# Optimization experiments

Hardware: AMD Instinct MI355X
Metric: run time of the kernel (lower is better)

The kernel has to match this reference:

```python
import jax, jax.numpy as jnp
import numpy as np

INPUT_SIZE = 1000
EMB = 1024          # 2**ceil(log2(input_size))
NQ = 10             # log2(EMB)
NL = 3              # n_qlayers (hardcoded in module)
B = 4096


def _rot(phi, theta, omega):
    # PennyLane qml.Rot(phi, theta, omega) = RZ(omega) RY(theta) RZ(phi)
    c = jnp.cos(theta * 0.5).astype(jnp.complex64)
    s = jnp.sin(theta * 0.5).astype(jnp.complex64)
    ea = jnp.exp(-0.5j * (phi + omega))   # e^{-i(phi+omega)/2}
    eb = jnp.exp(0.5j * (phi - omega))    # e^{ i(phi-omega)/2}
    row0 = jnp.stack([ea * c, -eb * s])
    row1 = jnp.stack([jnp.conj(eb) * s, jnp.conj(ea) * c])
    return jnp.stack([row0, row1])        # [2, 2] complex64


def _apply_1q(psi, U, q):
    # psi: [B] + [2]*NQ ; contract qubit axis q+1 with U
    psi = jnp.tensordot(psi, U, axes=[[q + 1], [1]])
    return jnp.moveaxis(psi, -1, q + 1)


def _apply_cnot(psi, c, t):
    c_ax, t_ax = c + 1, t + 1
    psi0 = jax.lax.index_in_dim(psi, 0, axis=c_ax, keepdims=False)
    psi1 = jax.lax.index_in_dim(psi, 1, axis=c_ax, keepdims=False)
    f_ax = t_ax - 1 if t_ax > c_ax else t_ax
    psi1 = jnp.flip(psi1, axis=f_ax)      # X on target when control=1
    return jnp.stack([psi0, psi1], axis=c_ax)


def _circuit(x, w):
    # AmplitudeEmbedding(normalize=True) + StronglyEntanglingLayers + probs
    norm = jnp.sqrt(jnp.sum(x * x, axis=1, keepdims=True))
    psi = (x / norm).astype(jnp.complex64)
    b = psi.shape[0]
    psi = psi.reshape((b,) + (2,) * NQ)   # wire 0 = most-significant bit
    for l in range(NL):
        for q in range(NQ):
            psi = _apply_1q(psi, _rot(w[l, q, 0], w[l, q, 1], w[l, q, 2]), q)
        r = l % (NQ - 1) + 1              # default SEL ranges
        for q in range(NQ):
            psi = _apply_cnot(psi, q, (q + r) % NQ)
    return (psi.real ** 2 + psi.imag ** 2).reshape(b, -1)  # probs [B, 2**NQ]


def setup_inputs() -> dict:
    key = jax.random.key(0)
    ks = jax.random.split(key, 12)
    d = {
        'inputs': jax.random.normal(ks[0], (B, INPUT_SIZE), jnp.float32),
        'weightsEnc': 0.1 * jax.random.normal(ks[1], (NL, NQ, 3), jnp.float32),
        'weightsDec': 0.1 * jax.random.normal(ks[2], (NL, NQ, 3), jnp.float32),
        'W0': jax.random.normal(ks[3], (INPUT_SIZE, EMB), jnp.float32) / np.sqrt(INPUT_SIZE),
        'b0': jnp.zeros((EMB,), jnp.float32),
        'W1': jax.random.normal(ks[4], (EMB, 2 * EMB), jnp.float32) / np.sqrt(EMB),
        'b1': jnp.zeros((2 * EMB,), jnp.float32),
        'W2': jax.random.normal(ks[5], (2 * EMB, EMB), jnp.float32) / np.sqrt(2 * EMB),
        'b2': jnp.zeros((EMB,), jnp.float32),
        'W3': jax.random.normal(ks[6], (EMB, INPUT_SIZE), jnp.float32) / np.sqrt(EMB),
        'b3': jnp.zeros((INPUT_SIZE,), jnp.float32),
    }
    return d


def reference(inputs, weightsEnc, weightsDec, W0, b0, W1, b1, W2, b2, W3, b3):
    x = inputs @ W0 + b0                 # Dense(embedding_dim)
    x = _circuit(x, weightsEnc)          # encoder qnode (vmapped over batch)
    x = x @ W1 + b1                      # Dense(2*embedding_dim)
    x = x @ W2 + b2                      # Dense(embedding_dim)
    x = _circuit(x, weightsDec)          # decoder qnode
    x = x @ W3 + b3                      # Dense(input_size)
    x = jnp.abs(x)
    return x / jnp.sum(x, axis=1, keepdims=True)
```

## Files before the change

kernel.cpp:

```cpp
#include <hip/hip_runtime.h>
#include <math.h>


#define B_SZ 4096
#define EMB 1024
#define NQ 10
#define NL 3

typedef __bf16 bf16x8 __attribute__((ext_vector_type(8)));
typedef float f32x4 __attribute__((ext_vector_type(4)));
typedef unsigned short u16x8 __attribute__((ext_vector_type(8)));

__device__ __forceinline__ unsigned short f2bf_rne(float f) {
    unsigned int u = __float_as_uint(f);
    u += 0x7FFFu + ((u >> 16) & 1u);
    return (unsigned short)(u >> 16);
}
__device__ __forceinline__ float bf2f(unsigned short h) {
    return __uint_as_float(((unsigned int)h) << 16);
}
__device__ __forceinline__ float lane_bcast(float v, int l) {
    return __uint_as_float(__builtin_amdgcn_readlane(__float_as_uint(v), l));
}

__device__ __forceinline__ void gll16(const void* g, void* l) {
    __builtin_amdgcn_global_load_lds(
        (const __attribute__((address_space(1))) void*)g,
        (__attribute__((address_space(3))) void*)l, 16, 0, 0);
}

#define GBM 128
#define GBN 128
#define GBK 32

__global__ __launch_bounds__(512) void gemm3_mfma(
    const unsigned short* __restrict__ Ah, const unsigned short* __restrict__ Al,
    const unsigned short* __restrict__ Bh, const unsigned short* __restrict__ Bl,
    const float* __restrict__ bias, float* __restrict__ C,
    int Kp, int Np, int Ksplit, size_t zStride)
{
    __shared__ __align__(16) char lds[32768];
    char* ldsAh = lds;
    char* ldsAl = lds + 8192;
    char* ldsBh = lds + 16384;
    char* ldsBl = lds + 24576;

    const int tid = threadIdx.x;
    const int lane = tid & 63;
    const int wv = tid >> 6;
    const int wm = wv >> 1;
    const int wn = wv & 1;
    const int blockRow = blockIdx.y * GBM;
    const int blockCol = blockIdx.x * GBN;
    const int z = blockIdx.z;

    const int srow = tid >> 2;
    const int skel = (tid & 3) * 8;
    const size_t aOff = ((size_t)(blockRow + srow) * Kp + skel + (size_t)z * Ksplit) * 2;
    const size_t bOff = ((size_t)(blockCol + srow) * Kp + skel + (size_t)z * Ksplit) * 2;
    const char* aHp = (const char*)Ah + aOff;
    const char* aLp = (const char*)Al + aOff;
    const char* bHp = (const char*)Bh + bOff;
    const char* bLp = (const char*)Bl + bOff;
    const int stageOff = wv * 1024;

    f32x4 acc[2][4];
    #pragma unroll
    for (int i = 0; i < 2; ++i)
        #pragma unroll
        for (int j = 0; j < 4; ++j)
            #pragma unroll
            for (int r = 0; r < 4; ++r) acc[i][j][r] = 0.f;

    const int kq = (lane >> 4) * 16;
    int aFragOff[2], bFragOff[4];
    #pragma unroll
    for (int i = 0; i < 2; ++i) aFragOff[i] = (wm * 32 + i * 16 + (lane & 15)) * 64 + kq;
    #pragma unroll
    for (int j = 0; j < 4; ++j) bFragOff[j] = (wn * 64 + j * 16 + (lane & 15)) * 64 + kq;

    const int nsteps = Ksplit / GBK;
    for (int s = 0; s < nsteps; ++s) {
        const size_t kb = (size_t)s * GBK * 2;
        gll16(aHp + kb, ldsAh + stageOff);
        gll16(aLp + kb, ldsAl + stageOff);
        gll16(bHp + kb, ldsBh + stageOff);
        gll16(bLp + kb, ldsBl + stageOff);
        __syncthreads();

        bf16x8 ah[2], al[2], bh[4], bl[4];
        #pragma unroll
        for (int i = 0; i < 2; ++i) {
            ah[i] = *(const bf16x8*)(ldsAh + aFragOff[i]);
            al[i] = *(const bf16x8*)(ldsAl + aFragOff[i]);
        }
        #pragma unroll
        for (int j = 0; j < 4; ++j) {
            bh[j] = *(const bf16x8*)(ldsBh + bFragOff[j]);
            bl[j] = *(const bf16x8*)(ldsBl + bFragOff[j]);
        }
        #pragma unroll
        for (int j = 0; j < 4; ++j)
            #pragma unroll
            for (int i = 0; i < 2; ++i) {
                acc[i][j] = __builtin_amdgcn_mfma_f32_16x16x32_bf16(al[i], bh[j], acc[i][j], 0, 0, 0);
                acc[i][j] = __builtin_amdgcn_mfma_f32_16x16x32_bf16(ah[i], bl[j], acc[i][j], 0, 0, 0);
                acc[i][j] = __builtin_amdgcn_mfma_f32_16x16x32_bf16(ah[i], bh[j], acc[i][j], 0, 0, 0);
            }
        __syncthreads();
    }

    float* Cz = C + (size_t)z * zStride;
    const bool addB = (z == 0) && (bias != nullptr);
    const int rquad = (lane >> 4) * 4;
    const int cidx = lane & 15;
    #pragma unroll
    for (int i = 0; i < 2; ++i)
        #pragma unroll
        for (int j = 0; j < 4; ++j) {
            #pragma unroll
            for (int r = 0; r < 4; ++r) {
                int row = blockRow + wm * 32 + i * 16 + rquad + r;
                int col = blockCol + wn * 64 + j * 16 + cidx;
                float v = acc[i][j][r];
                if (addB) v += bias[col];
                Cz[(size_t)row * Np + col] = v;
            }
        }
}

__global__ __launch_bounds__(256) void tsplit_kernel(
    const float* __restrict__ W, unsigned short* __restrict__ H, unsigned short* __restrict__ L,
    int K, int N, int Kp)
{
    __shared__ float tile[32][33];
    const int tid = threadIdx.x;
    const int tx = tid & 31, ty = tid >> 5;
    const int k0 = blockIdx.x * 32, n0 = blockIdx.y * 32;
    #pragma unroll
    for (int i = 0; i < 4; ++i) {
        int k = k0 + ty + i * 8, n = n0 + tx;
        tile[ty + i * 8][tx] = (k < K && n < N) ? W[(size_t)k * N + n] : 0.f;
    }
    __syncthreads();
    #pragma unroll
    for (int i = 0; i < 4; ++i) {
        int n = n0 + ty + i * 8, k = k0 + tx;
        float v = tile[tx][ty + i * 8];
        size_t o = (size_t)n * Kp + k;
        unsigned short h = f2bf_rne(v);
        H[o] = h;
        L[o] = f2bf_rne(v - bf2f(h));
    }
}

__global__ __launch_bounds__(256) void tsplit4_kernel(
    const float* __restrict__ P, unsigned short* __restrict__ H, unsigned short* __restrict__ L)
{
    __shared__ float tile[32][33];
    const int tid = threadIdx.x;
    const int tx = tid & 31, ty = tid >> 5;
    const int k0 = blockIdx.x * 32, n0 = blockIdx.y * 32;
    #pragma unroll
    for (int i = 0; i < 4; ++i) {
        int k = k0 + ty + i * 8, n = n0 + tx;
        size_t o = (size_t)k * 1024 + n;
        tile[ty + i * 8][tx] = P[o] + P[o + (1u << 20)] + P[o + (2u << 20)] + P[o + (3u << 20)];
    }
    __syncthreads();
    #pragma unroll
    for (int i = 0; i < 4; ++i) {
        int n = n0 + ty + i * 8, k = k0 + tx;
        float v = tile[tx][ty + i * 8];
        size_t o = (size_t)n * 1024 + k;
        unsigned short h = f2bf_rne(v);
        H[o] = h;
        L[o] = f2bf_rne(v - bf2f(h));
    }
}

__global__ __launch_bounds__(256) void split_rows_kernel(
    const float* __restrict__ X, unsigned short* __restrict__ H, unsigned short* __restrict__ L,
    int C, int Cp)
{
    const int r = blockIdx.x;
    for (int c = threadIdx.x; c < Cp; c += 256) {
        float v = (c < C) ? X[(size_t)r * C + c] : 0.f;
        unsigned short h = f2bf_rne(v);
        size_t o = (size_t)r * Cp + c;
        H[o] = h;
        L[o] = f2bf_rne(v - bf2f(h));
    }
}

__global__ void padbias_kernel(const float* __restrict__ b, float* __restrict__ bp, int N, int Np) {
    int i = blockIdx.x * 256 + threadIdx.x;
    if (i < Np) bp[i] = (i < N) ? b[i] : 0.f;
}

__global__ __launch_bounds__(256) void b12_kernel(
    const float* __restrict__ b1, const float* __restrict__ W2,
    const float* __restrict__ b2, float* __restrict__ b12)
{
    __shared__ float red[4][64];
    const int tx = threadIdx.x & 63;
    const int ty = threadIdx.x >> 6;
    const int n = blockIdx.x * 64 + tx;
    float s = 0.f;
    for (int j = ty * 512; j < (ty + 1) * 512; ++j)
        s += b1[j] * W2[(size_t)j * 1024 + n];
    red[ty][tx] = s;
    __syncthreads();
    if (ty == 0) b12[n] = red[0][tx] + red[1][tx] + red[2][tx] + red[3][tx] + b2[n];
}

__global__ void gatecoef_kernel(const float* __restrict__ wEnc,
                                const float* __restrict__ wDec,
                                float* __restrict__ G)
{
    int g = threadIdx.x;
    if (g >= 60) return;
    const float* w = (g < 30) ? (wEnc + g * 3) : (wDec + (g - 30) * 3);
    float* o = G + ((g < 30) ? g : (g - 30 + 64)) * 8;
    float phi = w[0], th = w[1], om = w[2];
    float ch = cosf(0.5f * th), sh = sinf(0.5f * th);
    float ap = 0.5f * (phi + om), am = 0.5f * (phi - om);
    float cap = cosf(ap), sap = sinf(ap);
    float cam = cosf(am), sam = sinf(am);
    o[0] =  cap * ch; o[1] = -sap * ch;
    o[2] = -cam * sh; o[3] = -sam * sh;
    o[4] =  cam * sh; o[5] = -sam * sh;
    o[6] =  cap * ch; o[7] =  sap * ch;
}


template<int GATE, int Q>
__device__ __forceinline__ void apply_rot(float (&xr)[16], float (&xi)[16],
                                          const float (&tbl)[8], int lane)
{
    float are = lane_bcast(tbl[0], GATE), aim = lane_bcast(tbl[1], GATE);
    float bre = lane_bcast(tbl[2], GATE), bim = lane_bcast(tbl[3], GATE);
    float cre = lane_bcast(tbl[4], GATE), cim = lane_bcast(tbl[5], GATE);
    float dre = lane_bcast(tbl[6], GATE), dim_ = lane_bcast(tbl[7], GATE);
    constexpr int S = 1 << (9 - Q);
    if constexpr (S < 16) {
        #pragma unroll
        for (int p = 0; p < 8; ++p) {
            int r0 = (p / S) * (2 * S) + (p % S);
            int r1 = r0 + S;
            float x0r = xr[r0], x0i = xi[r0], x1r = xr[r1], x1i = xi[r1];
            xr[r0] = are * x0r - aim * x0i + bre * x1r - bim * x1i;
            xi[r0] = are * x0i + aim * x0r + bre * x1i + bim * x1r;
            xr[r1] = cre * x0r - cim * x0i + dre * x1r - dim_ * x1i;
            xi[r1] = cre * x0i + cim * x0r + dre * x1i + dim_ * x1r;
        }
    } else {
        constexpr int M = S >> 4;
        bool bit = (lane & M) != 0;
        float pre = bit ? dre : are, pim = bit ? dim_ : aim;
        float qre = bit ? cre : bre, qim = bit ? cim : bim;
        #pragma unroll
        for (int r = 0; r < 16; ++r) {
            float ore = __shfl_xor(xr[r], M, 64);
            float oim = __shfl_xor(xi[r], M, 64);
            float nr = pre * xr[r] - pim * xi[r] + qre * ore - qim * oim;
            float ni = pre * xi[r] + pim * xr[r] + qre * oim + qim * ore;
            xr[r] = nr; xi[r] = ni;
        }
    }
}

template<int C, int T>
__device__ __forceinline__ void apply_cnot(float (&xr)[16], float (&xi)[16], int lane)
{
    constexpr int SC = 1 << (9 - C), ST = 1 << (9 - T);
    if constexpr (SC < 16 && ST < 16) {
        #pragma unroll
        for (int r = 0; r < 16; ++r) {
            if ((r & SC) && !(r & ST)) {
                int j = r | ST;
                float t;
                t = xr[r]; xr[r] = xr[j]; xr[j] = t;
                t = xi[r]; xi[r] = xi[j]; xi[j] = t;
            }
        }
    } else if constexpr (SC < 16) {
        constexpr int MT = ST >> 4;
        #pragma unroll
        for (int r = 0; r < 16; ++r) {
            if (r & SC) {
                xr[r] = __shfl_xor(xr[r], MT, 64);
                xi[r] = __shfl_xor(xi[r], MT, 64);
            }
        }
    } else if constexpr (ST < 16) {
        constexpr int MC = SC >> 4;
        bool bit = (lane & MC) != 0;
        #pragma unroll
        for (int r = 0; r < 16; ++r) {
            if (!(r & ST)) {
                int j = r | ST;
                float a0 = xr[r], a1 = xr[j];
                xr[r] = bit ? a1 : a0;  xr[j] = bit ? a0 : a1;
                float b0 = xi[r], b1 = xi[j];
                xi[r] = bit ? b1 : b0;  xi[j] = bit ? b0 : b1;
            }
        }
    } else {
        constexpr int MC = SC >> 4, MT = ST >> 4;
        bool bit = (lane & MC) != 0;
        #pragma unroll
        for (int r = 0; r < 16; ++r) {
            float o = __shfl_xor(xr[r], MT, 64);
            xr[r] = bit ? o : xr[r];
            float oi = __shfl_xor(xi[r], MT, 64);
            xi[r] = bit ? oi : xi[r];
        }
    }
}

template<int L, int Q>
__device__ __forceinline__ void rots(float (&xr)[16], float (&xi)[16],
                                     const float (&tbl)[8], int lane) {
    apply_rot<L * 10 + Q, Q>(xr, xi, tbl, lane);
    if constexpr (Q < 9) rots<L, Q + 1>(xr, xi, tbl, lane);
}
template<int L, int Q>
__device__ __forceinline__ void cnots(float (&xr)[16], float (&xi)[16], int lane) {
    constexpr int R = (L % 9) + 1;
    apply_cnot<Q, (Q + R) % 10>(xr, xi, lane);
    if constexpr (Q < 9) cnots<L, Q + 1>(xr, xi, lane);
}

__global__ __launch_bounds__(256, 4) void circuit_reg_kernel(
    const float* __restrict__ X0, const float* __restrict__ X1,
    unsigned short* __restrict__ Ph, unsigned short* __restrict__ Pl,
    const float* __restrict__ G)
{
    const int lane = threadIdx.x & 63;
    const int item = blockIdx.x * 4 + (threadIdx.x >> 6);
    const size_t base = (size_t)item * 1024 + lane * 16;

    float tbl[8];
    {
        const float4* gp = (const float4*)(G + lane * 8);
        float4 t0 = gp[0], t1 = gp[1];
        tbl[0] = t0.x; tbl[1] = t0.y; tbl[2] = t0.z; tbl[3] = t0.w;
        tbl[4] = t1.x; tbl[5] = t1.y; tbl[6] = t1.z; tbl[7] = t1.w;
    }

    float xr[16], xi[16];
    const float4* xb0 = (const float4*)(X0 + base);
    const float4* xb1 = (const float4*)(X1 + base);
    #pragma unroll
    for (int v = 0; v < 4; ++v) {
        float4 f = xb0[v], g = xb1[v];
        xr[v * 4 + 0] = f.x + g.x; xr[v * 4 + 1] = f.y + g.y;
        xr[v * 4 + 2] = f.z + g.z; xr[v * 4 + 3] = f.w + g.w;
    }
    #pragma unroll
    for (int r = 0; r < 16; ++r) xi[r] = 0.f;

    float nrm = 0.f;
    #pragma unroll
    for (int r = 0; r < 16; ++r) nrm += xr[r] * xr[r];
    #pragma unroll
    for (int m = 32; m >= 1; m >>= 1) nrm += __shfl_xor(nrm, m, 64);
    float inv = 1.0f / sqrtf(nrm);
    #pragma unroll
    for (int r = 0; r < 16; ++r) xr[r] *= inv;

    rots<0, 0>(xr, xi, tbl, lane);  cnots<0, 0>(xr, xi, lane);
    rots<1, 0>(xr, xi, tbl, lane);  cnots<1, 0>(xr, xi, lane);
    rots<2, 0>(xr, xi, tbl, lane);  cnots<2, 0>(xr, xi, lane);

    u16x8 h[2], lo[2];
    #pragma unroll
    for (int r = 0; r < 16; ++r) {
        float p = xr[r] * xr[r] + xi[r] * xi[r];
        unsigned short hh = f2bf_rne(p);
        h[r >> 3][r & 7] = hh;
        lo[r >> 3][r & 7] = f2bf_rne(p - bf2f(hh));
    }
    *(u16x8*)(Ph + base) = h[0];
    *(u16x8*)(Ph + base + 8) = h[1];
    *(u16x8*)(Pl + base) = lo[0];
    *(u16x8*)(Pl + base + 8) = lo[1];
}

__global__ __launch_bounds__(256) void absnorm_kernel(
    const float* __restrict__ X0, const float* __restrict__ X1,
    float* __restrict__ out, int N, int stride)
{
    __shared__ float red[4];
    const int row = blockIdx.x;
    const int tid = threadIdx.x;
    const float* x0 = X0 + (size_t)row * stride;
    const float* x1 = X1 + (size_t)row * stride;

    float s = 0.f;
    for (int i = tid; i < N; i += 256) s += fabsf(x0[i] + x1[i]);
    #pragma unroll
    for (int off = 32; off > 0; off >>= 1) s += __shfl_down(s, off);
    if ((tid & 63) == 0) red[tid >> 6] = s;
    __syncthreads();
    float inv = 1.0f / (red[0] + red[1] + red[2] + red[3]);
    for (int i = tid; i < N; i += 256)
        out[(size_t)row * N + i] = fabsf(x0[i] + x1[i]) * inv;
}

extern "C" void kernel_launch(void* const* d_in, const int* in_sizes, int n_in,
                              void* d_out, int out_size, void* d_ws, size_t ws_size,
                              hipStream_t stream)
{
    const float* inputs = (const float*)d_in[0];
    const float* wEnc   = (const float*)d_in[1];
    const float* wDec   = (const float*)d_in[2];
    const float* W0     = (const float*)d_in[3];
    const float* b0     = (const float*)d_in[4];
    const float* W1     = (const float*)d_in[5];
    const float* b1     = (const float*)d_in[6];
    const float* W2     = (const float*)d_in[7];
    const float* b2     = (const float*)d_in[8];
    const float* W3     = (const float*)d_in[9];
    const float* b3     = (const float*)d_in[10];
    float* out = (float*)d_out;

    char* w = (char*)d_ws;
    auto alloc = [&](size_t bytes) { char* p = w; w += (bytes + 255) & ~(size_t)255; return p; };

    unsigned short* Bt0h  = (unsigned short*)alloc((size_t)1024 * 1024 * 2);
    unsigned short* Bt0l  = (unsigned short*)alloc((size_t)1024 * 1024 * 2);
    unsigned short* Bt2h  = (unsigned short*)alloc((size_t)1024 * 2048 * 2);
    unsigned short* Bt2l  = (unsigned short*)alloc((size_t)1024 * 2048 * 2);
    unsigned short* Bt3h  = (unsigned short*)alloc((size_t)1024 * 1024 * 2);
    unsigned short* Bt3l  = (unsigned short*)alloc((size_t)1024 * 1024 * 2);
    unsigned short* Bt12h = (unsigned short*)alloc((size_t)1024 * 1024 * 2);
    unsigned short* Bt12l = (unsigned short*)alloc((size_t)1024 * 1024 * 2);
    unsigned short* W1h   = (unsigned short*)alloc((size_t)1024 * 2048 * 2);
    unsigned short* W1l   = (unsigned short*)alloc((size_t)1024 * 2048 * 2);
    float*          b3p   = (float*)alloc(1024 * 4);
    float*          b12   = (float*)alloc(1024 * 4);
    float*          G     = (float*)alloc(2 * 512 * 4);
    unsigned short* Ah    = (unsigned short*)alloc((size_t)B_SZ * 1024 * 2);
    unsigned short* Al    = (unsigned short*)alloc((size_t)B_SZ * 1024 * 2);
    unsigned short* ph    = (unsigned short*)alloc((size_t)B_SZ * 1024 * 2);
    unsigned short* pl    = (unsigned short*)alloc((size_t)B_SZ * 1024 * 2);
    float*          P     = (float*)alloc((size_t)2 * B_SZ * 1024 * 4);
    float* P12 = P;
    const size_t ZS = (size_t)B_SZ * 1024;

    dim3 blk256(256);

    tsplit_kernel<<<dim3(32, 32), blk256, 0, stream>>>(W0, Bt0h, Bt0l, 1000, 1024, 1024);
    tsplit_kernel<<<dim3(64, 32), blk256, 0, stream>>>(W2, Bt2h, Bt2l, 2048, 1024, 2048);
    tsplit_kernel<<<dim3(32, 32), blk256, 0, stream>>>(W3, Bt3h, Bt3l, 1024, 1000, 1024);
    split_rows_kernel<<<1024, blk256, 0, stream>>>(W1, W1h, W1l, 2048, 2048);
    padbias_kernel<<<4, blk256, 0, stream>>>(b3, b3p, 1000, 1024);
    b12_kernel<<<16, blk256, 0, stream>>>(b1, W2, b2, b12);
    gatecoef_kernel<<<1, 64, 0, stream>>>(wEnc, wDec, G);
    split_rows_kernel<<<B_SZ, blk256, 0, stream>>>(inputs, Ah, Al, 1000, 1024);

    gemm3_mfma<<<dim3(8, 8, 4), 512, 0, stream>>>(
        W1h, W1l, Bt2h, Bt2l, nullptr, P12, 2048, 1024, 512, (size_t)1 << 20);
    tsplit4_kernel<<<dim3(32, 32), blk256, 0, stream>>>(P12, Bt12h, Bt12l);

    gemm3_mfma<<<dim3(8, 32, 2), 512, 0, stream>>>(
        Ah, Al, Bt0h, Bt0l, b0, P, 1024, 1024, 512, ZS);
    circuit_reg_kernel<<<B_SZ / 4, blk256, 0, stream>>>(P, P + ZS, ph, pl, G);
    gemm3_mfma<<<dim3(8, 32, 2), 512, 0, stream>>>(
        ph, pl, Bt12h, Bt12l, b12, P, 1024, 1024, 512, ZS);
    circuit_reg_kernel<<<B_SZ / 4, blk256, 0, stream>>>(P, P + ZS, ph, pl, G + 512);
    gemm3_mfma<<<dim3(8, 32, 2), 512, 0, stream>>>(
        ph, pl, Bt3h, Bt3l, b3p, P, 1024, 1024, 512, ZS);
    absnorm_kernel<<<B_SZ, blk256, 0, stream>>>(P, P + ZS, out, 1000, 1024);
}
```

Before: 439.6 us.

## Merge prep kernels, use DPP/swizzle lane exchanges, deepen split-K for W1·W2

Merges the weight transpose/split kernels into one launch and the bias/gate-coefficient kernels into another, cutting launch count. Replaces __shfl_xor (ds_bpermute) in the quantum circuit kernel with DPP moves and ds_swizzle for small xor distances, which avoids the address computation and LDS-crossbar path. Raises the split-K factor of the W1·W2 precompute GEMM from 4 to 8 for more parallelism, and sums 8 partials in the follow-up kernel, which adds extra partial-buffer traffic.

```diff
diff --git a/kernel.cpp b/kernel.cpp
--- a/kernel.cpp
+++ b/kernel.cpp
@@ -21,6 +21,22 @@
 }
 __device__ __forceinline__ float lane_bcast(float v, int l) {
     return __uint_as_float(__builtin_amdgcn_readlane(__float_as_uint(v), l));
+}
+
+template<int M>
+__device__ __forceinline__ float lane_xor(float v) {
+    if constexpr (M == 1)
+        return __uint_as_float(__builtin_amdgcn_mov_dpp(__float_as_uint(v), 0xB1, 0xF, 0xF, true));
+    else if constexpr (M == 2)
+        return __uint_as_float(__builtin_amdgcn_mov_dpp(__float_as_uint(v), 0x4E, 0xF, 0xF, true));
+    else if constexpr (M == 8)
+        return __uint_as_float(__builtin_amdgcn_mov_dpp(__float_as_uint(v), 0x128, 0xF, 0xF, true));
+    else if constexpr (M == 4)
+        return __uint_as_float(__builtin_amdgcn_ds_swizzle(__float_as_uint(v), 0x101F));
+    else if constexpr (M == 16)
+        return __uint_as_float(__builtin_amdgcn_ds_swizzle(__float_as_uint(v), 0x401F));
+    else
+        return __shfl_xor(v, 32, 64);
 }
 
 __device__ __forceinline__ void gll16(const void* g, void* l) {
@@ -129,14 +145,13 @@
         }
 }
 
-__global__ __launch_bounds__(256) void tsplit_kernel(
+__device__ __forceinline__ void tsplit_block(
     const float* __restrict__ W, unsigned short* __restrict__ H, unsigned short* __restrict__ L,
-    int K, int N, int Kp)
+    int K, int N, int Kp, int bx, int by, int tid)
 {
     __shared__ float tile[32][33];
-    const int tid = threadIdx.x;
     const int tx = tid & 31, ty = tid >> 5;
-    const int k0 = blockIdx.x * 32, n0 = blockIdx.y * 32;
+    const int k0 = bx * 32, n0 = by * 32;
     #pragma unroll
     for (int i = 0; i < 4; ++i) {
         int k = k0 + ty + i * 8, n = n0 + tx;
@@ -154,7 +169,74 @@
     }
 }
 
-__global__ __launch_bounds__(256) void tsplit4_kernel(
+__global__ __launch_bounds__(256) void prep_weights_kernel(
+    const float* __restrict__ W0, unsigned short* __restrict__ Bt0h, unsigned short* __restrict__ Bt0l,
+    const float* __restrict__ W2, unsigned short* __restrict__ Bt2h, unsigned short* __restrict__ Bt2l,
+    const float* __restrict__ W3, unsigned short* __restrict__ Bt3h, unsigned short* __restrict__ Bt3l,
+    const float* __restrict__ W1, unsigned short* __restrict__ W1h, unsigned short* __restrict__ W1l)
+{
+    const int bid = blockIdx.x;
+    const int tid = threadIdx.x;
+    if (bid < 1024) {
+        tsplit_block(W0, Bt0h, Bt0l, 1000, 1024, 1024, bid & 31, bid >> 5, tid);
+    } else if (bid < 3072) {
+        int b = bid - 1024;
+        tsplit_block(W2, Bt2h, Bt2l, 2048, 1024, 2048, b & 63, b >> 6, tid);
+    } else if (bid < 4096) {
+        int b = bid - 3072;
+        tsplit_block(W3, Bt3h, Bt3l, 1024, 1000, 1024, b & 31, b >> 5, tid);
+    } else {
+        int r = bid - 4096;
+        for (int c = tid; c < 2048; c += 256) {
+            float v = W1[(size_t)r * 2048 + c];
+            unsigned short h = f2bf_rne(v);
+            size_t o = (size_t)r * 2048 + c;
+            W1h[o] = h;
+            W1l[o] = f2bf_rne(v - bf2f(h));
+        }
+    }
+}
+
+__global__ __launch_bounds__(256) void prep_misc_kernel(
+    const float* __restrict__ b1, const float* __restrict__ W2, const float* __restrict__ b2,
+    float* __restrict__ b12,
+    const float* __restrict__ b3, float* __restrict__ b3p,
+    const float* __restrict__ wEnc, const float* __restrict__ wDec, float* __restrict__ G)
+{
+    __shared__ float red[4][64];
+    const int bid = blockIdx.x;
+    const int tid = threadIdx.x;
+    if (bid < 16) {
+        const int tx = tid & 63, ty = tid >> 6;
+        const int n = bid * 64 + tx;
+        float s = 0.f;
+        for (int j = ty * 512; j < (ty + 1) * 512; ++j)
+            s += b1[j] * W2[(size_t)j * 1024 + n];
+        red[ty][tx] = s;
+        __syncthreads();
+        if (ty == 0) b12[n] = red[0][tx] + red[1][tx] + red[2][tx] + red[3][tx] + b2[n];
+    } else if (bid < 20) {
+        int i = (bid - 16) * 256 + tid;
+        b3p[i] = (i < 1000) ? b3[i] : 0.f;
+    } else {
+        int g = tid;
+        if (g < 60) {
+            const float* w = (g < 30) ? (wEnc + g * 3) : (wDec + (g - 30) * 3);
+            float* o = G + ((g < 30) ? g : (g - 30 + 64)) * 8;
+            float phi = w[0], th = w[1], om = w[2];
+            float ch = cosf(0.5f * th), sh = sinf(0.5f * th);
+            float ap = 0.5f * (phi + om), am = 0.5f * (phi - om);
+            float cap = cosf(ap), sap = sinf(ap);
+            float cam = cosf(am), sam = sinf(am);
+            o[0] =  cap * ch; o[1] = -sap * ch;
+            o[2] = -cam * sh; o[3] = -sam * sh;
+            o[4] =  cam * sh; o[5] = -sam * sh;
+            o[6] =  cap * ch; o[7] =  sap * ch;
+        }
+    }
+}
+
+__global__ __launch_bounds__(256) void tsplit8_kernel(
     const float* __restrict__ P, unsigned short* __restrict__ H, unsigned short* __restrict__ L)
 {
     __shared__ float tile[32][33];
@@ -165,7 +247,10 @@
     for (int i = 0; i < 4; ++i) {
         int k = k0 + ty + i * 8, n = n0 + tx;
         size_t o = (size_t)k * 1024 + n;
-        tile[ty + i * 8][tx] = P[o] + P[o + (1u << 20)] + P[o + (2u << 20)] + P[o + (3u << 20)];
+        float s = 0.f;
+        #pragma unroll
+        for (int zz = 0; zz < 8; ++zz) s += P[o + ((size_t)zz << 20)];
+        tile[ty + i * 8][tx] = s;
     }
     __syncthreads();
     #pragma unroll
@@ -191,46 +276,6 @@
         H[o] = h;
         L[o] = f2bf_rne(v - bf2f(h));
     }
-}
-
-__global__ void padbias_kernel(const float* __restrict__ b, float* __restrict__ bp, int N, int Np) {
-    int i = blockIdx.x * 256 + threadIdx.x;
-    if (i < Np) bp[i] = (i < N) ? b[i] : 0.f;
-}
-
-__global__ __launch_bounds__(256) void b12_kernel(
-    const float* __restrict__ b1, const float* __restrict__ W2,
-    const float* __restrict__ b2, float* __restrict__ b12)
-{
-    __shared__ float red[4][64];
-    const int tx = threadIdx.x & 63;
-    const int ty = threadIdx.x >> 6;
-    const int n = blockIdx.x * 64 + tx;
-    float s = 0.f;
-    for (int j = ty * 512; j < (ty + 1) * 512; ++j)
-        s += b1[j] * W2[(size_t)j * 1024 + n];
-    red[ty][tx] = s;
-    __syncthreads();
-    if (ty == 0) b12[n] = red[0][tx] + red[1][tx] + red[2][tx] + red[3][tx] + b2[n];
-}
-
-__global__ void gatecoef_kernel(const float* __restrict__ wEnc,
-                                const float* __restrict__ wDec,
-                                float* __restrict__ G)
-{
-    int g = threadIdx.x;
-    if (g >= 60) return;
-    const float* w = (g < 30) ? (wEnc + g * 3) : (wDec + (g - 30) * 3);
-    float* o = G + ((g < 30) ? g : (g - 30 + 64)) * 8;
-    float phi = w[0], th = w[1], om = w[2];
-    float ch = cosf(0.5f * th), sh = sinf(0.5f * th);
-    float ap = 0.5f * (phi + om), am = 0.5f * (phi - om);
-    float cap = cosf(ap), sap = sinf(ap);
-    float cam = cosf(am), sam = sinf(am);
-    o[0] =  cap * ch; o[1] = -sap * ch;
-    o[2] = -cam * sh; o[3] = -sam * sh;
-    o[4] =  cam * sh; o[5] = -sam * sh;
-    o[6] =  cap * ch; o[7] =  sap * ch;
 }
 
 
@@ -261,8 +306,8 @@
         float qre = bit ? cre : bre, qim = bit ? cim : bim;
         #pragma unroll
         for (int r = 0; r < 16; ++r) {
-            float ore = __shfl_xor(xr[r], M, 64);
-            float oim = __shfl_xor(xi[r], M, 64);
+            float ore = lane_xor<M>(xr[r]);
+            float oim = lane_xor<M>(xi[r]);
             float nr = pre * xr[r] - pim * xi[r] + qre * ore - qim * oim;
             float ni = pre * xi[r] + pim * xr[r] + qre * oim + qim * ore;
             xr[r] = nr; xi[r] = ni;
@@ -289,8 +334,8 @@
         #pragma unroll
         for (int r = 0; r < 16; ++r) {
             if (r & SC) {
-                xr[r] = __shfl_xor(xr[r], MT, 64);
-                xi[r] = __shfl_xor(xi[r], MT, 64);
+                xr[r] = lane_xor<MT>(xr[r]);
+                xi[r] = lane_xor<MT>(xi[r]);
             }
         }
     } else if constexpr (ST < 16) {
@@ -311,9 +356,9 @@
         bool bit = (lane & MC) != 0;
         #pragma unroll
         for (int r = 0; r < 16; ++r) {
-            float o = __shfl_xor(xr[r], MT, 64);
+            float o = lane_xor<MT>(xr[r]);
             xr[r] = bit ? o : xr[r];
-            float oi = __shfl_xor(xi[r], MT, 64);
+            float oi = lane_xor<MT>(xi[r]);
             xi[r] = bit ? oi : xi[r];
         }
     }
@@ -364,8 +409,12 @@
     float nrm = 0.f;
     #pragma unroll
     for (int r = 0; r < 16; ++r) nrm += xr[r] * xr[r];
-    #pragma unroll
-    for (int m = 32; m >= 1; m >>= 1) nrm += __shfl_xor(nrm, m, 64);
+    nrm += lane_xor<1>(nrm);
+    nrm += lane_xor<2>(nrm);
+    nrm += lane_xor<4>(nrm);
+    nrm += lane_xor<8>(nrm);
+    nrm += lane_xor<16>(nrm);
+    nrm += lane_xor<32>(nrm);
     float inv = 1.0f / sqrtf(nrm);
     #pragma unroll
     for (int r = 0; r < 16; ++r) xr[r] *= inv;
@@ -452,18 +501,14 @@
 
     dim3 blk256(256);
 
-    tsplit_kernel<<<dim3(32, 32), blk256, 0, stream>>>(W0, Bt0h, Bt0l, 1000, 1024, 1024);
-    tsplit_kernel<<<dim3(64, 32), blk256, 0, stream>>>(W2, Bt2h, Bt2l, 2048, 1024, 2048);
-    tsplit_kernel<<<dim3(32, 32), blk256, 0, stream>>>(W3, Bt3h, Bt3l, 1024, 1000, 1024);
-    split_rows_kernel<<<1024, blk256, 0, stream>>>(W1, W1h, W1l, 2048, 2048);
-    padbias_kernel<<<4, blk256, 0, stream>>>(b3, b3p, 1000, 1024);
-    b12_kernel<<<16, blk256, 0, stream>>>(b1, W2, b2, b12);
-    gatecoef_kernel<<<1, 64, 0, stream>>>(wEnc, wDec, G);
+    prep_weights_kernel<<<5120, blk256, 0, stream>>>(
+        W0, Bt0h, Bt0l, W2, Bt2h, Bt2l, W3, Bt3h, Bt3l, W1, W1h, W1l);
+    prep_misc_kernel<<<21, blk256, 0, stream>>>(b1, W2, b2, b12, b3, b3p, wEnc, wDec, G);
     split_rows_kernel<<<B_SZ, blk256, 0, stream>>>(inputs, Ah, Al, 1000, 1024);
 
-    gemm3_mfma<<<dim3(8, 8, 4), 512, 0, stream>>>(
-        W1h, W1l, Bt2h, Bt2l, nullptr, P12, 2048, 1024, 512, (size_t)1 << 20);
-    tsplit4_kernel<<<dim3(32, 32), blk256, 0, stream>>>(P12, Bt12h, Bt12l);
+    gemm3_mfma<<<dim3(8, 8, 8), 512, 0, stream>>>(
+        W1h, W1l, Bt2h, Bt2l, nullptr, P12, 2048, 1024, 256, (size_t)1 << 20);
+    tsplit8_kernel<<<dim3(32, 32), blk256, 0, stream>>>(P12, Bt12h, Bt12l);
 
     gemm3_mfma<<<dim3(8, 32, 2), 512, 0, stream>>>(
         Ah, Al, Bt0h, Bt0l, b0, P, 1024, 1024, 512, ZS);
```

Measured after the change: 413.4 us. 1.06x faster.
